# Kernel optimization log

Hardware: AMD Instinct MI355X
Metric: run time of the kernel (lower is better)

## Reference

```python
import jax, jax.numpy as jnp
import numpy as np

VOCAB = 32000
EMB = 256
HID = 1024
N = 5            # n-gram order
NM1 = N - 1      # context length
PAD = 0          # pad_index (ignore_index for CE, padding_idx for embedding)


def setup_inputs() -> dict:
    key = jax.random.key(0)
    ks = jax.random.split(key, 9)
    B, S = 16, 512
    text = jax.random.randint(ks[0], (B, S), 0, VOCAB)
    target = jax.random.randint(ks[1], (B, S), 0, VOCAB)
    sc = lambda fan_in: 1.0 / np.sqrt(fan_in)
    embed = jax.random.normal(ks[2], (VOCAB, EMB), jnp.float32) * 0.02
    W1 = jax.random.uniform(ks[3], (NM1 * EMB, HID), jnp.float32, -sc(NM1 * EMB), sc(NM1 * EMB))
    b1 = jax.random.uniform(ks[4], (HID,), jnp.float32, -sc(NM1 * EMB), sc(NM1 * EMB))
    W2 = jax.random.uniform(ks[5], (HID, HID), jnp.float32, -sc(HID), sc(HID))
    b2 = jax.random.uniform(ks[6], (HID,), jnp.float32, -sc(HID), sc(HID))
    Wo = jax.random.uniform(ks[7], (HID, VOCAB), jnp.float32, -sc(HID), sc(HID))
    bo = jax.random.uniform(ks[8], (VOCAB,), jnp.float32, -sc(HID), sc(HID))
    return {"text": text, "target": target, "embed": embed,
            "W1": W1, "b1": b1, "W2": W2, "b2": b2, "Wo": Wo, "bo": bo}


def reference(text, target, embed, W1, b1, W2, b2, Wo, bo):
    B, S = text.shape
    # left-pad with PAD so contexts[:, i] == previous n-1 tokens (padded for i < n-1)
    padded = jnp.pad(text, ((0, 0), (NM1, 0)), constant_values=PAD)  # [B, S+NM1]
    win = jnp.arange(S)[:, None] + jnp.arange(NM1)[None, :]          # [S, NM1]
    ctx = padded[:, win]                                             # [B, S, NM1]
    # nn.Embedding padding_idx: pad row is zero
    tab = embed.at[PAD].set(0.0)
    e = tab[ctx].reshape(B, S, NM1 * EMB)                            # [B, S, NM1*E]
    h1 = jax.nn.relu(jnp.einsum('bsd,dh->bsh', e, W1) + b1)
    h2 = jax.nn.relu(jnp.einsum('bsh,hk->bsk', h1, W2) + b2)
    logits = jnp.einsum('bsh,hv->bsv', h2, Wo) + bo                  # [B, S, V]
    logp = jax.nn.log_softmax(logits, axis=-1)
    nll = -jnp.take_along_axis(logp, target[..., None], axis=-1)[..., 0]  # [B, S]
    mask = (target != PAD).astype(logits.dtype)
    cnt = jnp.maximum(mask.sum(axis=0), 1.0)                         # per-timestep valid count
    step_loss = (nll * mask).sum(axis=0) / cnt                       # CE mean per step (ignore pad)
    return step_loss.mean()                                          # total_loss / seq_len
```

## Files before the change

kernel.cpp:

```cpp
#include <hip/hip_runtime.h>
#include <cstdint>
#include <cstddef>

#define VOCAB 32000
#define EMB   256
#define HID   1024
#define NB    16
#define SS    512
#define MTOK  (NB*SS)
#define KDIM  1024
#define NCHUNK 500
#define PSTRIDE 512

typedef __bf16 bf16_t;
typedef bf16_t bf16x8 __attribute__((ext_vector_type(8)));
typedef float  f32x4  __attribute__((ext_vector_type(4)));
typedef float  f32x16 __attribute__((ext_vector_type(16)));
typedef int    i32x4  __attribute__((ext_vector_type(4)));
typedef int    i32x8  __attribute__((ext_vector_type(8)));

__device__ __forceinline__ unsigned short f32_to_bf16(float f) {
  union { float f; unsigned int u; } v; v.f = f;
  unsigned int u = v.u;
  unsigned int r = (u + 0x7FFFu + ((u >> 16) & 1u)) >> 16;
  return (unsigned short)r;
}

__device__ __forceinline__ int f32_to_e2m1(float x) {
  int s = (x < 0.f) ? 8 : 0;
  float a = fabsf(x);
  int m;
  if      (a < 0.25f) m = 0;
  else if (a < 0.75f) m = 1;
  else if (a < 1.25f) m = 2;
  else if (a < 1.75f) m = 3;
  else if (a < 2.50f) m = 4;
  else if (a < 3.50f) m = 5;
  else if (a < 5.00f) m = 6;
  else                m = 7;
  return s | m;
}

__device__ __forceinline__ float e2m1_val(int c) {
  int m = c & 7;
  float mag = (m == 0) ? 0.0f : (m == 1) ? 0.5f : (m == 2) ? 1.0f :
              (m == 3) ? 1.5f : (m == 4) ? 2.0f : (m == 5) ? 3.0f :
              (m == 6) ? 4.0f : 6.0f;
  return (c & 8) ? -mag : mag;
}

__device__ __forceinline__ void gload_lds16(const void* gsrc, void* ldst) {
  __builtin_amdgcn_global_load_lds(
      (__attribute__((address_space(1))) void*)gsrc,
      (__attribute__((address_space(3))) void*)ldst,
      16, 0, 0);
}


__global__ void k_transpose_bf16(const float* __restrict__ in,
                                 unsigned short* __restrict__ out,
                                 int R, int C) {
  __shared__ float tile[32][33];
  int bc = blockIdx.x * 32, br = blockIdx.y * 32;
  int tx = threadIdx.x & 31, ty = threadIdx.x >> 5;
#pragma unroll
  for (int i = 0; i < 32; i += 8)
    tile[ty + i][tx] = in[(size_t)(br + ty + i) * C + (bc + tx)];
  __syncthreads();
#pragma unroll
  for (int i = 0; i < 32; i += 8)
    out[(size_t)(bc + ty + i) * R + (br + tx)] = f32_to_bf16(tile[tx][ty + i]);
}

__global__ void k_wo_frag(const float* __restrict__ Wo, uint8_t* __restrict__ Bf) {
  __shared__ uint8_t tile[64][128];
  const int v0 = blockIdx.x * 128, k0 = blockIdx.y * 64;
  const int tid = threadIdx.x;
#pragma unroll
  for (int rr = 0; rr < 8; ++rr) {
    int row = rr * 8 + (tid >> 5);
    const float4 f = *(const float4*)&Wo[(size_t)(k0 + row) * VOCAB + v0 + (tid & 31) * 4];
    int vb = (tid & 31) * 4;
    tile[row][vb + 0] = (uint8_t)f32_to_e2m1(f.x * 64.0f);
    tile[row][vb + 1] = (uint8_t)f32_to_e2m1(f.y * 64.0f);
    tile[row][vb + 2] = (uint8_t)f32_to_e2m1(f.z * 64.0f);
    tile[row][vb + 3] = (uint8_t)f32_to_e2m1(f.w * 64.0f);
  }
  __syncthreads();
  const int rec = tid >> 6, l = tid & 63;
  const int vloc = rec * 32 + (l & 31);
  const int kb = (l >> 5) * 32;
  uint8_t* out = Bf + ((size_t)((blockIdx.x * 4 + rec) * 16 + blockIdx.y)) * 1024 + l * 16;
  union { uint8_t b[16]; i32x4 v; } pk;
#pragma unroll
  for (int j = 0; j < 16; ++j)
    pk.b[j] = (uint8_t)(tile[kb + 2 * j][vloc] | (tile[kb + 2 * j + 1][vloc] << 4));
  *(i32x4*)(out) = pk.v;
}

__global__ void k_gather_e(const int* __restrict__ text,
                           const float* __restrict__ embed,
                           unsigned short* __restrict__ E) {
  int t = blockIdx.x;
  int b = t >> 9, s = t & 511;
  int d = threadIdx.x;
#pragma unroll
  for (int j = 0; j < 4; ++j) {
    int sidx = s + j - 4;
    int tok = (sidx >= 0) ? text[b * SS + sidx] : 0;
    float val = (tok != 0) ? embed[(size_t)tok * EMB + d] : 0.0f;
    E[(size_t)t * KDIM + j * EMB + d] = f32_to_bf16(val);
  }
}

template<int OUTQ>
__global__ __launch_bounds__(256)
void k_gemm_ffn(const unsigned short* __restrict__ A,
                const unsigned short* __restrict__ Bt,
                const float* __restrict__ bias,
                void* __restrict__ Hout, int N) {
  __shared__ unsigned short As[128 * 32];
  __shared__ unsigned short Bs[128 * 32];
  const int tid  = threadIdx.x;
  const int bn   = blockIdx.x, bm = blockIdx.y;
  const int lane = tid & 63, wid = tid >> 6;
  const int wm = wid >> 1, wn = wid & 1;
  const int g = lane >> 4, c = lane & 15;

  f32x4 acc[4][4];
#pragma unroll
  for (int m = 0; m < 4; ++m)
#pragma unroll
    for (int n = 0; n < 4; ++n) { f32x4 z = {0.f, 0.f, 0.f, 0.f}; acc[m][n] = z; }

  const int arow = tid >> 2;
  const int slotb = ((tid & 3) ^ ((tid >> 3) & 3)) * 16;
  const char* gA0 = (const char*)A + ((size_t)(bm * 128 + arow) * KDIM) * 2 + slotb;
  const char* gA1 = gA0 + (size_t)64 * KDIM * 2;
  const char* gB0 = (const char*)Bt + ((size_t)(bn * 128 + arow) * KDIM) * 2 + slotb;
  const char* gB1 = gB0 + (size_t)64 * KDIM * 2;
  char* lA = (char*)As + tid * 16;
  char* lB = (char*)Bs + tid * 16;

  const int rs = (g ^ ((c >> 1) & 3)) * 8;

  for (int kt = 0; kt < KDIM / 32; ++kt) {
    const int kb = kt * 64;
    gload_lds16(gA0 + kb, lA);
    gload_lds16(gA1 + kb, lA + 4096);
    gload_lds16(gB0 + kb, lB);
    gload_lds16(gB1 + kb, lB + 4096);
    __syncthreads();

    bf16x8 af[4], bf[4];
#pragma unroll
    for (int m = 0; m < 4; ++m)
      af[m] = *(const bf16x8*)&As[(wm * 64 + m * 16 + c) * 32 + rs];
#pragma unroll
    for (int n = 0; n < 4; ++n)
      bf[n] = *(const bf16x8*)&Bs[(wn * 64 + n * 16 + c) * 32 + rs];
#pragma unroll
    for (int m = 0; m < 4; ++m)
#pragma unroll
      for (int n = 0; n < 4; ++n)
        acc[m][n] = __builtin_amdgcn_mfma_f32_16x16x32_bf16(af[m], bf[n], acc[m][n], 0, 0, 0);
    __syncthreads();
  }

#pragma unroll
  for (int n = 0; n < 4; ++n) {
    int colg = bn * 128 + wn * 64 + n * 16 + c;
    float bv = bias[colg];
#pragma unroll
    for (int m = 0; m < 4; ++m)
#pragma unroll
      for (int j = 0; j < 4; ++j) {
        int rowg = bm * 128 + wm * 64 + m * 16 + g * 4 + j;
        float v = acc[m][n][j] + bv;
        v = v > 0.f ? v : 0.f;
        if constexpr (OUTQ == 0) {
          ((unsigned short*)Hout)[(size_t)rowg * N + colg] = f32_to_bf16(v);
        } else {
          int q = f32_to_e2m1(v * 8.0f);
          int qo = __shfl_xor(q, 1);
          if ((c & 1) == 0) {
            int ra = rowg >> 5, kt2 = colg >> 6;
            int l = (rowg & 31) + ((colg >> 5) & 1) * 32;
            size_t off = ((size_t)(ra * 16 + kt2)) * 1024 + l * 16 + ((colg & 31) >> 1);
            ((uint8_t*)Hout)[off] = (uint8_t)(q | (qo << 4));
          }
        }
      }
  }
}

__global__ void k_tlog(const uint8_t* __restrict__ Af, const uint8_t* __restrict__ Bf,
                       const int* __restrict__ target, const float* __restrict__ bo,
                       float* __restrict__ tlog) {
  const int r = blockIdx.x;
  const int l = threadIdx.x;
  const int tgt = target[r];
  const int ra = r >> 5, la = r & 31;
  const int rb = tgt >> 5, lb = tgt & 31;
  const int kt = l >> 2, half = (l & 2) ? 32 : 0, bofs = (l & 1) * 8;
  const uint8_t* pa = Af + ((size_t)(ra * 16 + kt)) * 1024 + (la + half) * 16 + bofs;
  const uint8_t* pb = Bf + ((size_t)(rb * 16 + kt)) * 1024 + (lb + half) * 16 + bofs;
  uint2 wa = *(const uint2*)pa;
  uint2 wb = *(const uint2*)pb;
  float s = 0.f;
#pragma unroll
  for (int j = 0; j < 8; ++j)
    s += e2m1_val((wa.x >> (4 * j)) & 0xF) * e2m1_val((wb.x >> (4 * j)) & 0xF);
#pragma unroll
  for (int j = 0; j < 8; ++j)
    s += e2m1_val((wa.y >> (4 * j)) & 0xF) * e2m1_val((wb.y >> (4 * j)) & 0xF);
#pragma unroll
  for (int st = 1; st < 64; st <<= 1) s += __shfl_xor(s, st);
  if (l == 0) tlog[r] = s * (1.0f / 512.0f) + bo[tgt];
}

#define DPP_ADD_ASM(e_, DPPCTL) do {                                        \
    float _t;                                                               \
    asm("v_add_f32_dpp %0, %1, %2 " DPPCTL " row_mask:0xf bank_mask:0xf"    \
        : "=v"(_t) : "v"(e_), "v"(e_));                                     \
    (e_) = _t;                                                              \
  } while (0)

__global__ __launch_bounds__(256, 2)
void k_gemm_vocab_mx(const uint8_t* __restrict__ Af,
                     const uint8_t* __restrict__ Bf,
                     const float* __restrict__ bias,
                     float* __restrict__ psum) {
  const int tid  = threadIdx.x;
  const int lane = tid & 63, wid = tid >> 6;
  const int wm = wid >> 1, wn = wid & 1;
  const int lr = lane & 31, kb = lane >> 5;

  const int t   = blockIdx.x;
  const int xcd = t & 7, i = t >> 3;
  const int bm  = xcd * 8 + (i & 7);
  const int bn  = i >> 3;

  f32x16 acc[2][2];
#pragma unroll
  for (int m = 0; m < 2; ++m)
#pragma unroll
    for (int n = 0; n < 2; ++n)
#pragma unroll
      for (int e = 0; e < 16; ++e) acc[m][n][e] = 0.f;

  const uint8_t* pa0 = Af + ((size_t)(bm * 4 + wm * 2 + 0) * 16) * 1024 + lane * 16;
  const uint8_t* pa1 = Af + ((size_t)(bm * 4 + wm * 2 + 1) * 16) * 1024 + lane * 16;
  const uint8_t* pb0 = Bf + ((size_t)(bn * 4 + wn * 2 + 0) * 16) * 1024 + lane * 16;
  const uint8_t* pb1 = Bf + ((size_t)(bn * 4 + wn * 2 + 1) * 16) * 1024 + lane * 16;

#pragma unroll 1
  for (int kt = 0; kt < 16; ++kt) {
    i32x4 a0q = *(const i32x4*)(pa0);
    i32x4 a1q = *(const i32x4*)(pa1);
    i32x4 b0q = *(const i32x4*)(pb0);
    i32x4 b1q = *(const i32x4*)(pb1);
    pa0 += 1024; pa1 += 1024; pb0 += 1024; pb1 += 1024;

    i32x8 a0 = __builtin_shufflevector(a0q, a0q, 0, 1, 2, 3, -1, -1, -1, -1);
    i32x8 a1 = __builtin_shufflevector(a1q, a1q, 0, 1, 2, 3, -1, -1, -1, -1);
    i32x8 b0 = __builtin_shufflevector(b0q, b0q, 0, 1, 2, 3, -1, -1, -1, -1);
    i32x8 b1 = __builtin_shufflevector(b1q, b1q, 0, 1, 2, 3, -1, -1, -1, -1);

    __builtin_amdgcn_s_setprio(1);
    acc[0][0] = __builtin_amdgcn_mfma_scale_f32_32x32x64_f8f6f4(
        a0, b0, acc[0][0], 4, 4, 0, 124, 0, 121);
    acc[0][1] = __builtin_amdgcn_mfma_scale_f32_32x32x64_f8f6f4(
        a0, b1, acc[0][1], 4, 4, 0, 124, 0, 121);
    acc[1][0] = __builtin_amdgcn_mfma_scale_f32_32x32x64_f8f6f4(
        a1, b0, acc[1][0], 4, 4, 0, 124, 0, 121);
    acc[1][1] = __builtin_amdgcn_mfma_scale_f32_32x32x64_f8f6f4(
        a1, b1, acc[1][1], 4, 4, 0, 124, 0, 121);
    __builtin_amdgcn_s_setprio(0);
  }

  const int chunk = bn * 2 + wn;
  const int colbase = bn * 128 + wn * 64;
  float bov0 = bias[colbase + lr];
  float bov1 = bias[colbase + 32 + lr];
#pragma unroll
  for (int m = 0; m < 2; ++m) {
#pragma unroll
    for (int reg = 0; reg < 16; ++reg) {
      int rowg = bm * 128 + wm * 64 + m * 32 + (reg & 3) + 8 * (reg >> 2) + 4 * kb;
      float e = __expf(acc[m][0][reg] + bov0) + __expf(acc[m][1][reg] + bov1);
      DPP_ADD_ASM(e, "quad_perm:[1,0,3,2]");
      DPP_ADD_ASM(e, "quad_perm:[2,3,0,1]");
      DPP_ADD_ASM(e, "row_half_mirror");
      DPP_ADD_ASM(e, "row_mirror");
      {
        union { float f; int i; } a_, b_;
        a_.f = e; b_.i = __builtin_amdgcn_ds_swizzle(a_.i, 0x401F); e += b_.f;
      }
      if (lr == 0) psum[(size_t)rowg * PSTRIDE + chunk] = e;
    }
  }
}

__global__ void k_reduce_nll(const float* __restrict__ psum,
                             const float* __restrict__ tlog,
                             float* __restrict__ nll) {
  int row = blockIdx.x;
  int lane = threadIdx.x;
  float L = 0.f;
  for (int ch = lane; ch < NCHUNK; ch += 64)
    L += psum[(size_t)row * PSTRIDE + ch];
#pragma unroll
  for (int s = 1; s < 64; s <<= 1) L += __shfl_xor(L, s);
  if (lane == 0) nll[row] = logf(L) - tlog[row];
}

__global__ void k_loss(const int* __restrict__ target,
                       const float* __restrict__ nll,
                       float* __restrict__ out) {
  __shared__ float red[SS];
  int s = threadIdx.x;
  float sl = 0.f, cnt = 0.f;
#pragma unroll
  for (int b = 0; b < NB; ++b) {
    int idx = b * SS + s;
    if (target[idx] != 0) { sl += nll[idx]; cnt += 1.f; }
  }
  red[s] = sl / fmaxf(cnt, 1.f);
  __syncthreads();
  for (int st = 256; st > 0; st >>= 1) {
    if (s < st) red[s] += red[s + st];
    __syncthreads();
  }
  if (s == 0) out[0] = red[0] / (float)SS;
}

extern "C" void kernel_launch(void* const* d_in, const int* in_sizes, int n_in,
                              void* d_out, int out_size, void* d_ws, size_t ws_size,
                              hipStream_t stream) {
  (void)in_sizes; (void)n_in; (void)out_size; (void)ws_size;
  const int*   text   = (const int*)d_in[0];
  const int*   target = (const int*)d_in[1];
  const float* embed  = (const float*)d_in[2];
  const float* W1     = (const float*)d_in[3];
  const float* b1     = (const float*)d_in[4];
  const float* W2     = (const float*)d_in[5];
  const float* b2     = (const float*)d_in[6];
  const float* Wo     = (const float*)d_in[7];
  const float* bo     = (const float*)d_in[8];
  float* out = (float*)d_out;
  char* ws = (char*)d_ws;

  const size_t SZ_E = (size_t)MTOK * KDIM * 2;
  unsigned short* E   = (unsigned short*)(ws);
  unsigned short* H1  = (unsigned short*)(ws + SZ_E);
  uint8_t*        H2Q = (uint8_t*)(ws + 2 * SZ_E);
  char* p = ws + 2 * SZ_E + (size_t)MTOK * KDIM;
  unsigned short* W1t = (unsigned short*)p;  p += (size_t)HID * HID * 2;
  unsigned short* W2t = (unsigned short*)p;  p += (size_t)HID * HID * 2;
  uint8_t*        WoQ = (uint8_t*)p;         p += (size_t)VOCAB * HID;
  float* tlog = (float*)p;                   p += (size_t)MTOK * 4;
  float* nll  = (float*)p;
  float* psum = (float*)H1;

  k_transpose_bf16<<<dim3(HID / 32, HID / 32), 256, 0, stream>>>(W1, W1t, HID, HID);
  k_transpose_bf16<<<dim3(HID / 32, HID / 32), 256, 0, stream>>>(W2, W2t, HID, HID);
  k_wo_frag<<<dim3(VOCAB / 128, HID / 64), 256, 0, stream>>>(Wo, WoQ);
  k_gather_e<<<MTOK, 256, 0, stream>>>(text, embed, E);

  k_gemm_ffn<0><<<dim3(HID / 128, MTOK / 128), 256, 0, stream>>>(E, W1t, b1, (void*)H1, HID);
  k_gemm_ffn<1><<<dim3(HID / 128, MTOK / 128), 256, 0, stream>>>(H1, W2t, b2, (void*)H2Q, HID);

  k_tlog<<<MTOK, 64, 0, stream>>>(H2Q, WoQ, target, bo, tlog);

  k_gemm_vocab_mx<<<dim3((MTOK / 128) * (VOCAB / 128)), 256, 0, stream>>>(
      H2Q, WoQ, bo, psum);

  k_reduce_nll<<<MTOK, 64, 0, stream>>>(psum, tlog, nll);
  k_loss<<<1, SS, 0, stream>>>(target, nll, out);
}
```

Baseline: 319.9 us.

## Switch FFN GEMMs to FP8 MX-scaled MFMA with pre-fragmented operand layouts

Replaces the bf16 LDS-tiled FFN GEMMs with FP8 (e4m3) scaled 32x32x64 MFMA kernels. Embeddings, W1 and W2 are quantized with a fixed power-of-two prescale directly into a register-fragment layout, so the GEMMs load operands from global memory without LDS staging. The first layer now writes FP8 fragments for the second, and block indices are remapped with an XCD-aware swizzle. This halves operand bytes and raises matrix throughput, at the cost of lower precision, which could move the loss away from the reference.

```diff
diff --git a/kernel.cpp b/kernel.cpp
--- a/kernel.cpp
+++ b/kernel.cpp
@@ -12,18 +12,33 @@
 #define NCHUNK 500
 #define PSTRIDE 512
 
-typedef __bf16 bf16_t;
-typedef bf16_t bf16x8 __attribute__((ext_vector_type(8)));
-typedef float  f32x4  __attribute__((ext_vector_type(4)));
 typedef float  f32x16 __attribute__((ext_vector_type(16)));
 typedef int    i32x4  __attribute__((ext_vector_type(4)));
 typedef int    i32x8  __attribute__((ext_vector_type(8)));
 
-__device__ __forceinline__ unsigned short f32_to_bf16(float f) {
-  union { float f; unsigned int u; } v; v.f = f;
-  unsigned int u = v.u;
-  unsigned int r = (u + 0x7FFFu + ((u >> 16) & 1u)) >> 16;
-  return (unsigned short)r;
+__device__ __forceinline__ uint8_t f32_to_e4m3(float x) {
+  union { float f; uint32_t u; } v; v.f = x;
+  uint32_t s = (v.u >> 24) & 0x80u;
+  int e = (int)((v.u >> 23) & 0xffu) - 127;
+  uint32_t m = v.u & 0x7fffffu;
+  if (e < -9) return (uint8_t)s;
+  if (e >= -6) {
+    uint32_t keep = m >> 20;
+    uint32_t rest = m & 0xfffffu;
+    keep += (rest > 0x80000u) || (rest == 0x80000u && (keep & 1u));
+    if (keep == 8u) { keep = 0u; e += 1; }
+    int code = ((e + 7) << 3) | (int)keep;
+    if (code >= 0x7f) code = 0x7e;
+    return (uint8_t)(s | (uint32_t)code);
+  }
+  uint32_t full = 0x800000u | m;
+  int shift = 20 + (-6 - e);
+  uint32_t keep = full >> shift;
+  uint32_t rest = full & ((1u << shift) - 1u);
+  uint32_t half = 1u << (shift - 1);
+  keep += (rest > half) || (rest == half && (keep & 1u));
+  if (keep >= 8u) return (uint8_t)(s | 0x08u);
+  return (uint8_t)(s | keep);
 }
 
 __device__ __forceinline__ int f32_to_e2m1(float x) {
@@ -49,27 +64,34 @@
   return (c & 8) ? -mag : mag;
 }
 
-__device__ __forceinline__ void gload_lds16(const void* gsrc, void* ldst) {
-  __builtin_amdgcn_global_load_lds(
-      (__attribute__((address_space(1))) void*)gsrc,
-      (__attribute__((address_space(3))) void*)ldst,
-      16, 0, 0);
-}
-
-
-__global__ void k_transpose_bf16(const float* __restrict__ in,
-                                 unsigned short* __restrict__ out,
-                                 int R, int C) {
-  __shared__ float tile[32][33];
-  int bc = blockIdx.x * 32, br = blockIdx.y * 32;
-  int tx = threadIdx.x & 31, ty = threadIdx.x >> 5;
-#pragma unroll
-  for (int i = 0; i < 32; i += 8)
-    tile[ty + i][tx] = in[(size_t)(br + ty + i) * C + (bc + tx)];
+
+__global__ void k_w_frag8(const float* __restrict__ W, uint8_t* __restrict__ Bf, int C) {
+  __shared__ uint8_t tile[64][128];
+  const int v0 = blockIdx.x * 128, k0 = blockIdx.y * 64;
+  const int tid = threadIdx.x;
+#pragma unroll
+  for (int rr = 0; rr < 8; ++rr) {
+    int row = rr * 8 + (tid >> 5);
+    const float4 f = *(const float4*)&W[(size_t)(k0 + row) * C + v0 + (tid & 31) * 4];
+    int vb = (tid & 31) * 4;
+    tile[row][vb + 0] = f32_to_e4m3(f.x * 16.0f);
+    tile[row][vb + 1] = f32_to_e4m3(f.y * 16.0f);
+    tile[row][vb + 2] = f32_to_e4m3(f.z * 16.0f);
+    tile[row][vb + 3] = f32_to_e4m3(f.w * 16.0f);
+  }
   __syncthreads();
-#pragma unroll
-  for (int i = 0; i < 32; i += 8)
-    out[(size_t)(bc + ty + i) * R + (br + tx)] = f32_to_bf16(tile[tx][ty + i]);
+  const int rec = tid >> 6, l = tid & 63;
+  const int vloc = rec * 32 + (l & 31);
+  const int kb = (l >> 5) * 32;
+  uint8_t* out = Bf + ((size_t)((blockIdx.x * 4 + rec) * 16 + blockIdx.y)) * 2048 + l * 16;
+  union { uint8_t b[16]; i32x4 v; } lo, hi;
+#pragma unroll
+  for (int j = 0; j < 16; ++j) {
+    lo.b[j] = tile[kb + j][vloc];
+    hi.b[j] = tile[kb + 16 + j][vloc];
+  }
+  *(i32x4*)(out)        = lo.v;
+  *(i32x4*)(out + 1024) = hi.v;
 }
 
 __global__ void k_wo_frag(const float* __restrict__ Wo, uint8_t* __restrict__ Bf) {
@@ -98,99 +120,121 @@
   *(i32x4*)(out) = pk.v;
 }
 
-__global__ void k_gather_e(const int* __restrict__ text,
-                           const float* __restrict__ embed,
-                           unsigned short* __restrict__ E) {
-  int t = blockIdx.x;
-  int b = t >> 9, s = t & 511;
-  int d = threadIdx.x;
-#pragma unroll
-  for (int j = 0; j < 4; ++j) {
-    int sidx = s + j - 4;
-    int tok = (sidx >= 0) ? text[b * SS + sidx] : 0;
-    float val = (tok != 0) ? embed[(size_t)tok * EMB + d] : 0.0f;
-    E[(size_t)t * KDIM + j * EMB + d] = f32_to_bf16(val);
-  }
-}
-
-template<int OUTQ>
-__global__ __launch_bounds__(256)
-void k_gemm_ffn(const unsigned short* __restrict__ A,
-                const unsigned short* __restrict__ Bt,
-                const float* __restrict__ bias,
-                void* __restrict__ Hout, int N) {
-  __shared__ unsigned short As[128 * 32];
-  __shared__ unsigned short Bs[128 * 32];
+__global__ void k_gather_frag8(const int* __restrict__ text,
+                               const float* __restrict__ embed,
+                               uint8_t* __restrict__ Af) {
+  const int rb = blockIdx.x, kt = blockIdx.y;
+  const int l = threadIdx.x;
+  const int t = rb * 32 + (l & 31);
+  const int b = t >> 9, s = t & 511;
+  const int j = kt >> 2;
+  const int sidx = s + j - 4;
+  const int tok = (sidx >= 0) ? text[b * SS + sidx] : 0;
+  uint8_t* out = Af + ((size_t)(rb * 16 + kt)) * 2048 + l * 16;
+  if (tok == 0) {
+    i32x4 z = {0, 0, 0, 0};
+    *(i32x4*)(out) = z;
+    *(i32x4*)(out + 1024) = z;
+    return;
+  }
+  const int d0 = (kt & 3) * 64 + (l >> 5) * 32;
+  const float* src = embed + (size_t)tok * EMB + d0;
+  union { uint8_t b[16]; i32x4 v; } lo, hi;
+#pragma unroll
+  for (int q = 0; q < 4; ++q) {
+    float4 f = *(const float4*)(src + q * 4);
+    lo.b[q * 4 + 0] = f32_to_e4m3(f.x * 16.0f);
+    lo.b[q * 4 + 1] = f32_to_e4m3(f.y * 16.0f);
+    lo.b[q * 4 + 2] = f32_to_e4m3(f.z * 16.0f);
+    lo.b[q * 4 + 3] = f32_to_e4m3(f.w * 16.0f);
+    float4 g = *(const float4*)(src + 16 + q * 4);
+    hi.b[q * 4 + 0] = f32_to_e4m3(g.x * 16.0f);
+    hi.b[q * 4 + 1] = f32_to_e4m3(g.y * 16.0f);
+    hi.b[q * 4 + 2] = f32_to_e4m3(g.z * 16.0f);
+    hi.b[q * 4 + 3] = f32_to_e4m3(g.w * 16.0f);
+  }
+  *(i32x4*)(out)        = lo.v;
+  *(i32x4*)(out + 1024) = hi.v;
+}
+
+template<int EPI>
+__global__ __launch_bounds__(256, 2)
+void k_gemm_mx8(const uint8_t* __restrict__ Af, const uint8_t* __restrict__ Bf,
+                const float* __restrict__ bias, uint8_t* __restrict__ Hq) {
   const int tid  = threadIdx.x;
-  const int bn   = blockIdx.x, bm = blockIdx.y;
   const int lane = tid & 63, wid = tid >> 6;
   const int wm = wid >> 1, wn = wid & 1;
-  const int g = lane >> 4, c = lane & 15;
-
-  f32x4 acc[4][4];
-#pragma unroll
-  for (int m = 0; m < 4; ++m)
-#pragma unroll
-    for (int n = 0; n < 4; ++n) { f32x4 z = {0.f, 0.f, 0.f, 0.f}; acc[m][n] = z; }
-
-  const int arow = tid >> 2;
-  const int slotb = ((tid & 3) ^ ((tid >> 3) & 3)) * 16;
-  const char* gA0 = (const char*)A + ((size_t)(bm * 128 + arow) * KDIM) * 2 + slotb;
-  const char* gA1 = gA0 + (size_t)64 * KDIM * 2;
-  const char* gB0 = (const char*)Bt + ((size_t)(bn * 128 + arow) * KDIM) * 2 + slotb;
-  const char* gB1 = gB0 + (size_t)64 * KDIM * 2;
-  char* lA = (char*)As + tid * 16;
-  char* lB = (char*)Bs + tid * 16;
-
-  const int rs = (g ^ ((c >> 1) & 3)) * 8;
-
-  for (int kt = 0; kt < KDIM / 32; ++kt) {
-    const int kb = kt * 64;
-    gload_lds16(gA0 + kb, lA);
-    gload_lds16(gA1 + kb, lA + 4096);
-    gload_lds16(gB0 + kb, lB);
-    gload_lds16(gB1 + kb, lB + 4096);
-    __syncthreads();
-
-    bf16x8 af[4], bf[4];
-#pragma unroll
-    for (int m = 0; m < 4; ++m)
-      af[m] = *(const bf16x8*)&As[(wm * 64 + m * 16 + c) * 32 + rs];
-#pragma unroll
-    for (int n = 0; n < 4; ++n)
-      bf[n] = *(const bf16x8*)&Bs[(wn * 64 + n * 16 + c) * 32 + rs];
-#pragma unroll
-    for (int m = 0; m < 4; ++m)
-#pragma unroll
-      for (int n = 0; n < 4; ++n)
-        acc[m][n] = __builtin_amdgcn_mfma_f32_16x16x32_bf16(af[m], bf[n], acc[m][n], 0, 0, 0);
-    __syncthreads();
-  }
-
-#pragma unroll
-  for (int n = 0; n < 4; ++n) {
-    int colg = bn * 128 + wn * 64 + n * 16 + c;
-    float bv = bias[colg];
-#pragma unroll
-    for (int m = 0; m < 4; ++m)
-#pragma unroll
-      for (int j = 0; j < 4; ++j) {
-        int rowg = bm * 128 + wm * 64 + m * 16 + g * 4 + j;
-        float v = acc[m][n][j] + bv;
-        v = v > 0.f ? v : 0.f;
-        if constexpr (OUTQ == 0) {
-          ((unsigned short*)Hout)[(size_t)rowg * N + colg] = f32_to_bf16(v);
-        } else {
-          int q = f32_to_e2m1(v * 8.0f);
-          int qo = __shfl_xor(q, 1);
-          if ((c & 1) == 0) {
-            int ra = rowg >> 5, kt2 = colg >> 6;
-            int l = (rowg & 31) + ((colg >> 5) & 1) * 32;
-            size_t off = ((size_t)(ra * 16 + kt2)) * 1024 + l * 16 + ((colg & 31) >> 1);
-            ((uint8_t*)Hout)[off] = (uint8_t)(q | (qo << 4));
-          }
+  const int lr = lane & 31, kb = lane >> 5;
+
+  const int o   = blockIdx.x;
+  const int xcd = o & 7, i = o >> 3;
+  const int bm  = xcd * 8 + (i & 7);
+  const int bn  = i >> 3;
+
+  f32x16 acc[2][2];
+#pragma unroll
+  for (int m = 0; m < 2; ++m)
+#pragma unroll
+    for (int n = 0; n < 2; ++n)
+#pragma unroll
+      for (int e = 0; e < 16; ++e) acc[m][n][e] = 0.f;
+
+  const uint8_t* pa0 = Af + ((size_t)(bm * 4 + wm * 2 + 0) * 16) * 2048 + lane * 16;
+  const uint8_t* pa1 = Af + ((size_t)(bm * 4 + wm * 2 + 1) * 16) * 2048 + lane * 16;
+  const uint8_t* pb0 = Bf + ((size_t)(bn * 4 + wn * 2 + 0) * 16) * 2048 + lane * 16;
+  const uint8_t* pb1 = Bf + ((size_t)(bn * 4 + wn * 2 + 1) * 16) * 2048 + lane * 16;
+
+#pragma unroll 1
+  for (int kt = 0; kt < 16; ++kt) {
+    i32x4 a0l = *(const i32x4*)(pa0), a0h = *(const i32x4*)(pa0 + 1024);
+    i32x4 a1l = *(const i32x4*)(pa1), a1h = *(const i32x4*)(pa1 + 1024);
+    i32x4 b0l = *(const i32x4*)(pb0), b0h = *(const i32x4*)(pb0 + 1024);
+    i32x4 b1l = *(const i32x4*)(pb1), b1h = *(const i32x4*)(pb1 + 1024);
+    pa0 += 2048; pa1 += 2048; pb0 += 2048; pb1 += 2048;
+
+    i32x8 a0 = __builtin_shufflevector(a0l, a0h, 0, 1, 2, 3, 4, 5, 6, 7);
+    i32x8 a1 = __builtin_shufflevector(a1l, a1h, 0, 1, 2, 3, 4, 5, 6, 7);
+    i32x8 b0 = __builtin_shufflevector(b0l, b0h, 0, 1, 2, 3, 4, 5, 6, 7);
+    i32x8 b1 = __builtin_shufflevector(b1l, b1h, 0, 1, 2, 3, 4, 5, 6, 7);
+
+    __builtin_amdgcn_s_setprio(1);
+    acc[0][0] = __builtin_amdgcn_mfma_scale_f32_32x32x64_f8f6f4(
+        a0, b0, acc[0][0], 0, 0, 0, 123, 0, 123);
+    acc[0][1] = __builtin_amdgcn_mfma_scale_f32_32x32x64_f8f6f4(
+        a0, b1, acc[0][1], 0, 0, 0, 123, 0, 123);
+    acc[1][0] = __builtin_amdgcn_mfma_scale_f32_32x32x64_f8f6f4(
+        a1, b0, acc[1][0], 0, 0, 0, 123, 0, 123);
+    acc[1][1] = __builtin_amdgcn_mfma_scale_f32_32x32x64_f8f6f4(
+        a1, b1, acc[1][1], 0, 0, 0, 123, 0, 123);
+    __builtin_amdgcn_s_setprio(0);
+  }
+
+  const int colbase = bn * 128 + wn * 64;
+  const int recc = colbase >> 6;
+  float bv0 = bias[colbase + lr];
+  float bv1 = bias[colbase + 32 + lr];
+#pragma unroll
+  for (int m = 0; m < 2; ++m) {
+#pragma unroll
+    for (int reg = 0; reg < 16; ++reg) {
+      int rowg = bm * 128 + wm * 64 + m * 32 + (reg & 3) + 8 * (reg >> 2) + 4 * kb;
+      float v0 = acc[m][0][reg] + bv0; v0 = v0 > 0.f ? v0 : 0.f;
+      float v1 = acc[m][1][reg] + bv1; v1 = v1 > 0.f ? v1 : 0.f;
+      size_t rec = (size_t)((rowg >> 5) * 16 + recc);
+      if constexpr (EPI == 0) {
+        size_t base = rec * 2048 + ((lr & 16) ? 1024 : 0) + (lr & 15);
+        Hq[base + (size_t)(rowg & 31) * 16]        = f32_to_e4m3(v0 * 16.0f);
+        Hq[base + (size_t)((rowg & 31) + 32) * 16] = f32_to_e4m3(v1 * 16.0f);
+      } else {
+        int q0 = f32_to_e2m1(v0 * 8.0f), q1 = f32_to_e2m1(v1 * 8.0f);
+        int q0o = __shfl_xor(q0, 1), q1o = __shfl_xor(q1, 1);
+        if ((lr & 1) == 0) {
+          size_t base = rec * 1024 + (lr >> 1);
+          Hq[base + (size_t)(rowg & 31) * 16]        = (uint8_t)(q0 | (q0o << 4));
+          Hq[base + (size_t)((rowg & 31) + 32) * 16] = (uint8_t)(q1 | (q1o << 4));
         }
       }
+    }
   }
 }
 
@@ -351,25 +395,24 @@
   float* out = (float*)d_out;
   char* ws = (char*)d_ws;
 
-  const size_t SZ_E = (size_t)MTOK * KDIM * 2;
-  unsigned short* E   = (unsigned short*)(ws);
-  unsigned short* H1  = (unsigned short*)(ws + SZ_E);
-  uint8_t*        H2Q = (uint8_t*)(ws + 2 * SZ_E);
-  char* p = ws + 2 * SZ_E + (size_t)MTOK * KDIM;
-  unsigned short* W1t = (unsigned short*)p;  p += (size_t)HID * HID * 2;
-  unsigned short* W2t = (unsigned short*)p;  p += (size_t)HID * HID * 2;
-  uint8_t*        WoQ = (uint8_t*)p;         p += (size_t)VOCAB * HID;
-  float* tlog = (float*)p;                   p += (size_t)MTOK * 4;
+  char* p = ws;
+  uint8_t* EQ  = (uint8_t*)p; p += (size_t)MTOK * KDIM;
+  uint8_t* H1Q = (uint8_t*)p; p += (size_t)MTOK * HID;
+  uint8_t* H2Q = (uint8_t*)p; p += (size_t)MTOK * HID / 2;
+  uint8_t* W1Q = (uint8_t*)p; p += (size_t)HID * HID;
+  uint8_t* W2Q = (uint8_t*)p; p += (size_t)HID * HID;
+  uint8_t* WoQ = (uint8_t*)p; p += (size_t)VOCAB * HID / 2;
+  float* psum = (float*)p;    p += (size_t)MTOK * PSTRIDE * 4;
+  float* tlog = (float*)p;    p += (size_t)MTOK * 4;
   float* nll  = (float*)p;
-  float* psum = (float*)H1;
-
-  k_transpose_bf16<<<dim3(HID / 32, HID / 32), 256, 0, stream>>>(W1, W1t, HID, HID);
-  k_transpose_bf16<<<dim3(HID / 32, HID / 32), 256, 0, stream>>>(W2, W2t, HID, HID);
+
+  k_w_frag8<<<dim3(HID / 128, HID / 64), 256, 0, stream>>>(W1, W1Q, HID);
+  k_w_frag8<<<dim3(HID / 128, HID / 64), 256, 0, stream>>>(W2, W2Q, HID);
   k_wo_frag<<<dim3(VOCAB / 128, HID / 64), 256, 0, stream>>>(Wo, WoQ);
-  k_gather_e<<<MTOK, 256, 0, stream>>>(text, embed, E);
-
-  k_gemm_ffn<0><<<dim3(HID / 128, MTOK / 128), 256, 0, stream>>>(E, W1t, b1, (void*)H1, HID);
-  k_gemm_ffn<1><<<dim3(HID / 128, MTOK / 128), 256, 0, stream>>>(H1, W2t, b2, (void*)H2Q, HID);
+  k_gather_frag8<<<dim3(MTOK / 32, 16), 64, 0, stream>>>(text, embed, EQ);
+
+  k_gemm_mx8<0><<<dim3((MTOK / 128) * (HID / 128)), 256, 0, stream>>>(EQ, W1Q, b1, H1Q);
+  k_gemm_mx8<1><<<dim3((MTOK / 128) * (HID / 128)), 256, 0, stream>>>(H1Q, W2Q, b2, H2Q);
 
   k_tlog<<<MTOK, 64, 0, stream>>>(H2Q, WoQ, target, bo, tlog);
 
```

Result: faster. 311.9 us (-2.5%).
